# Optimization experiments

Measured on AMD Instinct MI355X. Metric: run time of the kernel, lower is better.

## Reference

```python
import jax, jax.numpy as jnp
import numpy as np

H = 8          # heads
D = 512        # d_model
DK = D // H    # per-head dim
FF = 2048      # feed-forward size
STACKS = 3
VOCAB = 5000
PAD = 0
LN_EPS = 1e-6


def _layer_norm(x, g, b):
    mu = jnp.mean(x, axis=-1, keepdims=True)
    var = jnp.mean(jnp.square(x - mu), axis=-1, keepdims=True)
    return (x - mu) * jax.lax.rsqrt(var + LN_EPS) * g + b


def _positional_encoding(T, d):
    pos = jnp.arange(T, dtype=jnp.float32)[:, None]                      # (T,1)
    div = jnp.exp(jnp.arange(0, d, 2, dtype=jnp.float32) * (-np.log(10000.0) / d))
    pe = jnp.zeros((T, d), dtype=jnp.float32)
    pe = pe.at[:, 0::2].set(jnp.sin(pos * div))
    pe = pe.at[:, 1::2].set(jnp.cos(pos * div))
    return pe  # (T, D)


def _mha(q_in, kv, wq, bq, wk, bk, wv, bv, wo, bo, mask):
    B, Tq, _ = q_in.shape
    Tk = kv.shape[1]
    q = (q_in @ wq + bq).reshape(B, Tq, H, DK).transpose(0, 2, 1, 3)   # (B,H,Tq,DK)
    k = (kv @ wk + bk).reshape(B, Tk, H, DK).transpose(0, 2, 1, 3)
    v = (kv @ wv + bv).reshape(B, Tk, H, DK).transpose(0, 2, 1, 3)
    score = jnp.einsum('bhqd,bhkd->bhqk', q, k) / jnp.sqrt(jnp.float32(DK))
    if mask is not None:
        score = jnp.where(mask, score, jnp.float32(-1e9))
    p = jax.nn.softmax(score, axis=-1)
    out = jnp.einsum('bhqk,bhkd->bhqd', p, v)
    out = out.transpose(0, 2, 1, 3).reshape(B, Tq, D)
    return out @ wo + bo


def setup_inputs() -> dict:
    key = jax.random.key(0)
    ks = jax.random.split(key, 24)
    s = 0.02
    inp = {
        'target': jax.random.randint(ks[0], (32, 256), 0, VOCAB),
        'memory': jax.random.normal(ks[1], (32, 1024, D), dtype=jnp.float32),
        'emb': jax.random.normal(ks[2], (VOCAB, D), dtype=jnp.float32) * s,
        'ln_g': jnp.ones((D,), jnp.float32),
        'ln_b': jnp.zeros((D,), jnp.float32),
        'ff_w1': jax.random.normal(ks[3], (D, FF), jnp.float32) * s,
        'ff_b1': jnp.zeros((FF,), jnp.float32),
        'ff_w2': jax.random.normal(ks[4], (FF, D), jnp.float32) * s,
        'ff_b2': jnp.zeros((D,), jnp.float32),
    }
    names = ['wq', 'wk', 'wv', 'wo']
    for i, n in enumerate(names):
        inp['sa_' + n] = jax.random.normal(ks[5 + i], (D, D), jnp.float32) * s
        inp['sa_b' + n[1]] = jnp.zeros((D,), jnp.float32)
        inp['ca_' + n] = jax.random.normal(ks[9 + i], (D, D), jnp.float32) * s
        inp['ca_b' + n[1]] = jnp.zeros((D,), jnp.float32)
    return inp


def reference(target, memory, emb, ln_g, ln_b, ff_w1, ff_b1, ff_w2, ff_b2,
              sa_wq, sa_bq, sa_wk, sa_bk, sa_wv, sa_bv, sa_wo, sa_bo,
              ca_wq, ca_bq, ca_wk, ca_bk, ca_wv, ca_bv, ca_wo, ca_bo):
    B, T = target.shape
    x = emb[target] * jnp.sqrt(jnp.float32(D))              # (B,T,D)
    x = x + _positional_encoding(T, D)                       # dropout = identity (eval)
    # masks: causal & pad for self-attn; cross-attn mask is all-ones -> skip
    pad = (target != PAD)[:, None, :, None]                  # (B,1,T,1)
    causal = jnp.tril(jnp.ones((T, T), dtype=bool))          # (T,T)
    tgt_mask = pad & causal                                  # (B,1,T,T)
    out = x
    for _ in range(STACKS):  # shared parameters
        n = _layer_norm(out, ln_g, ln_b)
        out = out + _mha(n, n, sa_wq, sa_bq, sa_wk, sa_bk, sa_wv, sa_bv, sa_wo, sa_bo, tgt_mask)
        n = _layer_norm(out, ln_g, ln_b)
        out = out + _mha(n, memory, ca_wq, ca_bq, ca_wk, ca_bk, ca_wv, ca_bv, ca_wo, ca_bo, None)
        n = _layer_norm(out, ln_g, ln_b)
        out = out + (jax.nn.relu(n @ ff_w1 + ff_b1) @ ff_w2 + ff_b2)
    return _layer_norm(out, ln_g, ln_b)
```

## Files before the change

### kernel.cpp

```cpp
#include <hip/hip_runtime.h>
#include <cstdint>
#include <cstddef>

typedef unsigned short u16;
typedef __bf16 bf16x8 __attribute__((ext_vector_type(8)));
typedef float f32x4 __attribute__((ext_vector_type(4)));

#define DEV static __device__ __forceinline__

#define QSCALE 0.18033688011112042f

DEV u16 f2bf(float f) { unsigned v; __builtin_memcpy(&v, &f, 4); v += 0x7fffu + ((v >> 16) & 1u); return (u16)(v >> 16); }

DEV void gll16(const void* g, void* l) {
    __builtin_amdgcn_global_load_lds(
        (__attribute__((address_space(1))) void*)g,
        (__attribute__((address_space(3))) void*)l, 16, 0, 0);
}

__global__ void embed_pe(const int* __restrict__ tgt, const float* __restrict__ emb,
                         float* __restrict__ x)
{
    const int bt = blockIdx.x;
    const int t  = bt & 255;
    const int tok = tgt[bt];
    for (int d = threadIdx.x; d < 512; d += 256) {
        float e  = emb[(size_t)tok * 512 + d] * 22.62741699796952f;
        int   d0 = d & ~1;
        float ang = (float)t * expf((float)d0 * (-9.210340371976184f / 512.f));
        float pe  = (d & 1) ? cosf(ang) : sinf(ang);
        x[(size_t)bt * 512 + d] = e + pe;
    }
}

__global__ void transpose_k(const float* __restrict__ in, u16* __restrict__ out,
                            int K, int N)
{
    int id = blockIdx.x * 256 + threadIdx.x;
    int k = id / N, n = id % N;
    out[(size_t)n * K + k] = f2bf(in[id]);
}

__global__ void memcast(const float* __restrict__ in, u16* __restrict__ out)
{
    int i = (blockIdx.x * 256 + threadIdx.x) * 4;
    float4 v = *(const float4*)(in + i);
    uint2 w;
    w.x = (unsigned)f2bf(v.x) | ((unsigned)f2bf(v.y) << 16);
    w.y = (unsigned)f2bf(v.z) | ((unsigned)f2bf(v.w) << 16);
    *(uint2*)(out + i) = w;
}

__global__ void concat_bias(const float* __restrict__ a, const float* __restrict__ b,
                            float* __restrict__ out)
{
    int i = blockIdx.x * 256 + threadIdx.x;
    if (i < 512) { out[i] = a[i]; out[512 + i] = b[i]; }
}

template<bool OUTF32>
__global__ void layernorm_k(const float* __restrict__ x, const float* __restrict__ g,
                            const float* __restrict__ b, void* __restrict__ outv)
{
    const int row  = blockIdx.x * 4 + (threadIdx.x >> 6);
    const int lane = threadIdx.x & 63;
    const float* xr = x + (size_t)row * 512;
    float4 v0 = *(const float4*)(xr + lane * 4);
    float4 v1 = *(const float4*)(xr + 256 + lane * 4);
    float s = v0.x + v0.y + v0.z + v0.w + v1.x + v1.y + v1.z + v1.w;
    float q = v0.x*v0.x + v0.y*v0.y + v0.z*v0.z + v0.w*v0.w
            + v1.x*v1.x + v1.y*v1.y + v1.z*v1.z + v1.w*v1.w;
#pragma unroll
    for (int o = 1; o < 64; o <<= 1) { s += __shfl_xor(s, o, 64); q += __shfl_xor(q, o, 64); }
    float mu  = s * (1.f / 512.f);
    float var = q * (1.f / 512.f) - mu * mu;
    float rs  = rsqrtf(fmaxf(var, 0.f) + 1e-6f);

#pragma unroll
    for (int h = 0; h < 2; h++) {
        const int d0 = h * 256 + lane * 4;
        float4 v = h ? v1 : v0;
        float4 gg = *(const float4*)(g + d0);
        float4 bb = *(const float4*)(b + d0);
        float o0 = (v.x - mu) * rs * gg.x + bb.x;
        float o1 = (v.y - mu) * rs * gg.y + bb.y;
        float o2 = (v.z - mu) * rs * gg.z + bb.z;
        float o3 = (v.w - mu) * rs * gg.w + bb.w;
        if (OUTF32) {
            *(float4*)((float*)outv + (size_t)row * 512 + d0) = make_float4(o0, o1, o2, o3);
        } else {
            uint2 w;
            w.x = (unsigned)f2bf(o0) | ((unsigned)f2bf(o1) << 16);
            w.y = (unsigned)f2bf(o2) | ((unsigned)f2bf(o3) << 16);
            *(uint2*)((u16*)outv + (size_t)row * 512 + d0) = w;
        }
    }
}

template<bool OUTF32>
__global__ void ln_sum_k(const float* __restrict__ x, const float* __restrict__ p,
                         const float* __restrict__ g, const float* __restrict__ b,
                         float* __restrict__ xout, void* __restrict__ outv)
{
    const int row  = blockIdx.x * 4 + (threadIdx.x >> 6);
    const int lane = threadIdx.x & 63;
    const size_t base = (size_t)row * 512;
    const float* xr = x + base;
    const float* pa = p + base;
    const float* pb = p + 4194304 + base;
    float4 v0, v1;
    {
        float4 a = *(const float4*)(xr + lane * 4);
        float4 c = *(const float4*)(pa + lane * 4);
        float4 d = *(const float4*)(pb + lane * 4);
        v0 = make_float4(a.x + c.x + d.x, a.y + c.y + d.y, a.z + c.z + d.z, a.w + c.w + d.w);
        a = *(const float4*)(xr + 256 + lane * 4);
        c = *(const float4*)(pa + 256 + lane * 4);
        d = *(const float4*)(pb + 256 + lane * 4);
        v1 = make_float4(a.x + c.x + d.x, a.y + c.y + d.y, a.z + c.z + d.z, a.w + c.w + d.w);
    }
    float s = v0.x + v0.y + v0.z + v0.w + v1.x + v1.y + v1.z + v1.w;
    float q = v0.x*v0.x + v0.y*v0.y + v0.z*v0.z + v0.w*v0.w
            + v1.x*v1.x + v1.y*v1.y + v1.z*v1.z + v1.w*v1.w;
#pragma unroll
    for (int o = 1; o < 64; o <<= 1) { s += __shfl_xor(s, o, 64); q += __shfl_xor(q, o, 64); }
    float mu  = s * (1.f / 512.f);
    float var = q * (1.f / 512.f) - mu * mu;
    float rs  = rsqrtf(fmaxf(var, 0.f) + 1e-6f);

#pragma unroll
    for (int h = 0; h < 2; h++) {
        const int d0 = h * 256 + lane * 4;
        float4 v = h ? v1 : v0;
        if (!OUTF32) *(float4*)(xout + base + d0) = v;
        float4 gg = *(const float4*)(g + d0);
        float4 bb = *(const float4*)(b + d0);
        float o0 = (v.x - mu) * rs * gg.x + bb.x;
        float o1 = (v.y - mu) * rs * gg.y + bb.y;
        float o2 = (v.z - mu) * rs * gg.z + bb.z;
        float o3 = (v.w - mu) * rs * gg.w + bb.w;
        if (OUTF32) {
            *(float4*)((float*)outv + base + d0) = make_float4(o0, o1, o2, o3);
        } else {
            uint2 w;
            w.x = (unsigned)f2bf(o0) | ((unsigned)f2bf(o1) << 16);
            w.y = (unsigned)f2bf(o2) | ((unsigned)f2bf(o3) << 16);
            *(uint2*)((u16*)outv + base + d0) = w;
        }
    }
}

template<int EPI, bool BROW, int BN, int QS, int SPLIT>
__launch_bounds__(256, BN == 64 ? 4 : 2)
__global__ void gemm_bt(const u16* __restrict__ A, int lda,
                        const u16* __restrict__ Bt,
                        const float* __restrict__ bias,
                        void* __restrict__ outp, int ldo, int K)
{
    constexpr int NJ = BN / 32;
    __shared__ u16 As[2][128 * 32];
    __shared__ u16 Bs[2][BN * 32];

    const int gx = gridDim.x, gy = gridDim.y;
    const int nwg = gx * gy * gridDim.z;
    int lin = blockIdx.x + gx * (blockIdx.y + gy * blockIdx.z);
    lin = (lin & 7) * (nwg >> 3) + (lin >> 3);
    const int bx = lin % gx;
    const int rem = lin / gx;
    const int by = rem % gy;
    const int bz = rem / gy;

    const int tid  = threadIdx.x;
    const int lane = tid & 63;
    const int wave = tid >> 6;
    const int quad = lane >> 4, l16 = lane & 15;
    const int l4 = lane >> 2, c8 = (lane & 3) * 8;
    const int m0 = by * 128, n0 = bx * BN;
    const int wm = (wave >> 1) * 64, wn = (wave & 1) * (BN / 2);

    const int kc = K / SPLIT;
    const int kbeg = bz * kc;
    const int nsteps = kc / 32;

    f32x4 acc[4][NJ];
#pragma unroll
    for (int i = 0; i < 4; i++)
#pragma unroll
        for (int j = 0; j < NJ; j++) acc[i][j] = f32x4{0.f, 0.f, 0.f, 0.f};

#define GSTAGE(buf, kk)                                                                      \
    {                                                                                        \
        gll16(&A[(size_t)(m0 + wave * 32 + l4)      * lda + (kk) + c8], &As[buf][(wave * 32) * 32]);      \
        gll16(&A[(size_t)(m0 + wave * 32 + 16 + l4) * lda + (kk) + c8], &As[buf][(wave * 32 + 16) * 32]); \
        if (BN == 128) {                                                                     \
            gll16(&Bt[(size_t)(n0 + wave * 32 + l4)      * K + (kk) + c8], &Bs[buf][(wave * 32) * 32]);      \
            gll16(&Bt[(size_t)(n0 + wave * 32 + 16 + l4) * K + (kk) + c8], &Bs[buf][(wave * 32 + 16) * 32]); \
        } else {                                                                             \
            gll16(&Bt[(size_t)(n0 + wave * 16 + l4) * K + (kk) + c8], &Bs[buf][(wave * 16) * 32]);           \
        }                                                                                    \
    }

    GSTAGE(0, kbeg)
    __syncthreads();

    for (int st = 0; st < nsteps; st++) {
        const int cur = st & 1;
        if (st + 1 < nsteps) GSTAGE(cur ^ 1, kbeg + (st + 1) * 32)

        bf16x8 af[4], bfr[NJ];
#pragma unroll
        for (int i = 0; i < 4; i++) af[i]  = *(const bf16x8*)&As[cur][(wm + i * 16 + l16) * 32 + quad * 8];
#pragma unroll
        for (int j = 0; j < NJ; j++) bfr[j] = *(const bf16x8*)&Bs[cur][(wn + j * 16 + l16) * 32 + quad * 8];
#pragma unroll
        for (int i = 0; i < 4; i++)
#pragma unroll
            for (int j = 0; j < NJ; j++)
                acc[i][j] = __builtin_amdgcn_mfma_f32_16x16x32_bf16(af[i], bfr[j], acc[i][j], 0, 0, 0);

        __syncthreads();
    }
#undef GSTAGE

    const bool dobias = (SPLIT == 1) || (bz == 0);
#pragma unroll
    for (int i = 0; i < 4; i++)
#pragma unroll
        for (int j = 0; j < NJ; j++) {
            const int col = n0 + wn + j * 16 + l16;
            const float bc = BROW ? 0.f : (dobias ? bias[col] : 0.f);
#pragma unroll
            for (int r = 0; r < 4; r++) {
                const int row = m0 + wm + i * 16 + quad * 4 + r;
                const float bv = BROW ? (dobias ? bias[row] : 0.f) : bc;
                float v = acc[i][j][r] + bv;
                if (QS == 1) v *= QSCALE;
                if (QS == 2 && col < 512) v *= QSCALE;
                if (EPI == 1) v = fmaxf(v, 0.f);
                if (EPI == 3) {
                    ((float*)outp)[(size_t)bz * 8192 * ldo + (size_t)row * ldo + col] = v;
                } else {
                    ((u16*)outp)[(size_t)row * ldo + col] = f2bf(v);
                }
            }
        }
}

template<bool SELF>
__launch_bounds__(512, 4)
__global__ void attn(const u16* __restrict__ Qb, int qs,
                     const u16* __restrict__ Kb, int ks, int koff,
                     const u16* __restrict__ Vt, int ldv,
                     const int* __restrict__ target,
                     u16* __restrict__ Ob, int Tk)
{
    __shared__ u16 KV[2][4][64 * 32];
    __shared__ __align__(16) __bf16 P16[8][16 * 72];
    __shared__ int needtail;
    const int tid  = threadIdx.x;
    const int lane = tid & 63;
    const int wave = tid >> 6;
    const int quad = lane >> 4, l16 = lane & 15;
    const int b = blockIdx.x, h = blockIdx.y, qz = blockIdx.z;
    const int qbase = qz * 128 + wave * 16;
    const int hq = h * 64;
    const int kcol = ((quad ^ ((l16 >> 1) & 3)) * 8);

    if (tid == 0) needtail = 0;

    const u16* qr = Qb + (size_t)(b * 256 + qbase + l16) * qs + hq;
    bf16x8 qf0 = *(const bf16x8*)(qr + quad * 8);
    bf16x8 qf1 = *(const bf16x8*)(qr + 32 + quad * 8);

    f32x4 o[4];
#pragma unroll
    for (int t = 0; t < 4; t++) o[t] = f32x4{0.f, 0.f, 0.f, 0.f};
    float pr[4] = {0.f, 0.f, 0.f, 0.f};

    bool rv[4];
    bool tpad = false;
    if (SELF) {
        bool inv = false;
#pragma unroll
        for (int r = 0; r < 4; r++) {
            rv[r] = (target[b * 256 + qbase + quad * 4 + r] != 0);
            inv |= !rv[r];
        }
        tpad = __any(inv);
    }

    const u16* kbase = Kb + (size_t)b * Tk * ks + koff + hq;
    const u16* vbase = Vt + (size_t)hq * ldv + (size_t)b * Tk;
    __bf16* pw = P16[wave];

    const int srow0 = ((wave * 2) & 3) * 16 + (lane >> 2);
    const int srow1 = ((wave * 2 + 1) & 3) * 16 + (lane >> 2);
    const int sc0 = (((lane & 3) ^ ((srow0 >> 1) & 3)) * 8);
    const int sc1 = (((lane & 3) ^ ((srow1 >> 1) & 3)) * 8);
    const int arr0 = (wave * 2) >> 2, arr1 = (wave * 2 + 1) >> 2;
    u16* ldst0;  u16* ldst1;

#define STAGE_KV(buf, k0)                                                        \
    {                                                                            \
        const u16* src0; const u16* src1;                                        \
        if (arr0 == 0)      src0 = kbase + (size_t)((k0) + srow0) * ks + sc0;    \
        else if (arr0 == 1) src0 = kbase + (size_t)((k0) + srow0) * ks + 32 + sc0;\
        else if (arr0 == 2) src0 = vbase + (size_t)srow0 * ldv + (k0) + sc0;     \
        else                src0 = vbase + (size_t)srow0 * ldv + (k0) + 32 + sc0;\
        if (arr1 == 0)      src1 = kbase + (size_t)((k0) + srow1) * ks + sc1;    \
        else if (arr1 == 1) src1 = kbase + (size_t)((k0) + srow1) * ks + 32 + sc1;\
        else if (arr1 == 2) src1 = vbase + (size_t)srow1 * ldv + (k0) + sc1;     \
        else                src1 = vbase + (size_t)srow1 * ldv + (k0) + 32 + sc1;\
        ldst0 = &KV[buf][arr0][(((wave * 2) & 3) * 16) * 32];                    \
        ldst1 = &KV[buf][arr1][(((wave * 2 + 1) & 3) * 16) * 32];                \
        gll16(src0, ldst0);                                                      \
        gll16(src1, ldst1);                                                      \
    }

    STAGE_KV(0, 0)
    __syncthreads();
    if (SELF && tpad && lane == 0) needtail = 1;
    __syncthreads();
    const int nch = SELF ? (needtail ? (Tk >> 6) : 2 * (qz + 1)) : (Tk >> 6);

    for (int c = 0; c < nch; c++) {
        const int cur = c & 1;
        const int k0 = c * 64;
        if (c + 1 < nch) STAGE_KV(cur ^ 1, (c + 1) * 64)

        const u16* KsLc = KV[cur][0];
        const u16* KsHc = KV[cur][1];
        const u16* VsLc = KV[cur][2];
        const u16* VsHc = KV[cur][3];

        const bool active = !SELF || (qbase + 16 > k0) || tpad;
        if (active) {
#pragma unroll
            for (int g = 0; g < 4; g++) {
                bf16x8 kf0 = *(const bf16x8*)&KsLc[(g * 16 + l16) * 32 + kcol];
                bf16x8 kf1 = *(const bf16x8*)&KsHc[(g * 16 + l16) * 32 + kcol];
                f32x4 sv = f32x4{0.f, 0.f, 0.f, 0.f};
                sv = __builtin_amdgcn_mfma_f32_16x16x32_bf16(qf0, kf0, sv, 0, 0, 0);
                sv = __builtin_amdgcn_mfma_f32_16x16x32_bf16(qf1, kf1, sv, 0, 0, 0);
                if (SELF) {
                    if (k0 + 64 > qbase) {
#pragma unroll
                        for (int r = 0; r < 4; r++)
                            if (k0 + g * 16 + l16 > qbase + quad * 4 + r) sv[r] = -1e9f;
                    }
                    if (tpad) {
#pragma unroll
                        for (int r = 0; r < 4; r++)
                            if (!rv[r]) sv[r] = 0.f;
                    }
                }
#pragma unroll
                for (int r = 0; r < 4; r++) {
                    float p = exp2f(sv[r]);
                    pr[r] += p;
                    pw[(quad * 4 + r) * 72 + g * 16 + l16] = (__bf16)p;
                }
            }
            bf16x8 pa0 = *(const bf16x8*)&pw[l16 * 72 + quad * 8];
            bf16x8 pa1 = *(const bf16x8*)&pw[l16 * 72 + 32 + quad * 8];
#pragma unroll
            for (int t = 0; t < 4; t++) {
                bf16x8 vf0 = *(const bf16x8*)&VsLc[(t * 16 + l16) * 32 + kcol];
                bf16x8 vf1 = *(const bf16x8*)&VsHc[(t * 16 + l16) * 32 + kcol];
                o[t] = __builtin_amdgcn_mfma_f32_16x16x32_bf16(pa0, vf0, o[t], 0, 0, 0);
                o[t] = __builtin_amdgcn_mfma_f32_16x16x32_bf16(pa1, vf1, o[t], 0, 0, 0);
            }
        }
        __syncthreads();
    }
#undef STAGE_KV

#pragma unroll
    for (int r = 0; r < 4; r++) {
#pragma unroll
        for (int off = 1; off < 16; off <<= 1) pr[r] += __shfl_xor(pr[r], off, 64);
    }
#pragma unroll
    for (int r = 0; r < 4; r++) {
        const float inv_l = 1.f / pr[r];
        const int tq = qbase + quad * 4 + r;
        u16* orow = Ob + (size_t)(b * 256 + tq) * 512 + hq;
#pragma unroll
        for (int t = 0; t < 4; t++) orow[t * 16 + l16] = f2bf(o[t][r] * inv_l);
    }
}

#define O_X      ((size_t)0)
#define O_N      ((size_t)16777216)
#define O_QK     ((size_t)25165824)
#define O_VTS    ((size_t)41943040)
#define O_ATT    ((size_t)50331648)
#define O_FFN    ((size_t)58720256)
#define O_KVC    ((size_t)92274688)
#define O_VTC    ((size_t)125829120)
#define O_WQKT   ((size_t)159383552)
#define O_SAVT   ((size_t)160432128)
#define O_WOT    ((size_t)160956416)
#define O_CAQT   ((size_t)161480704)
#define O_CAKT   ((size_t)162004992)
#define O_CAVT   ((size_t)162529280)
#define O_CAWOT  ((size_t)163053568)
#define O_FF1T   ((size_t)163577856)
#define O_FF2T   ((size_t)165675008)
#define O_BQK    ((size_t)167772160)

extern "C" void kernel_launch(void* const* d_in, const int* in_sizes, int n_in,
                              void* d_out, int out_size, void* d_ws, size_t ws_size,
                              hipStream_t stream)
{
    const int*   target = (const int*)d_in[0];
    const float* memory = (const float*)d_in[1];
    const float* emb    = (const float*)d_in[2];
    const float* ln_g   = (const float*)d_in[3];
    const float* ln_b   = (const float*)d_in[4];
    const float* ff_w1  = (const float*)d_in[5];
    const float* ff_b1  = (const float*)d_in[6];
    const float* ff_w2  = (const float*)d_in[7];
    const float* ff_b2  = (const float*)d_in[8];
    const float* sa_wq  = (const float*)d_in[9];
    const float* sa_bq  = (const float*)d_in[10];
    const float* ca_wq  = (const float*)d_in[11];
    const float* ca_bq  = (const float*)d_in[12];
    const float* sa_wk  = (const float*)d_in[13];
    const float* sa_bk  = (const float*)d_in[14];
    const float* ca_wk  = (const float*)d_in[15];
    const float* ca_bk  = (const float*)d_in[16];
    const float* sa_wv  = (const float*)d_in[17];
    const float* sa_bv  = (const float*)d_in[18];
    const float* ca_wv  = (const float*)d_in[19];
    const float* ca_bv  = (const float*)d_in[20];
    const float* sa_wo  = (const float*)d_in[21];
    const float* sa_bo  = (const float*)d_in[22];
    const float* ca_wo  = (const float*)d_in[23];
    const float* ca_bo  = (const float*)d_in[24];

    char* ws = (char*)d_ws;
    float* xf   = (float*)(ws + O_X);
    u16* nbuf   = (u16*)(ws + O_N);
    u16* qk     = (u16*)(ws + O_QK);
    u16* qbuf   = (u16*)(ws + O_QK);
    float* ffp  = (float*)(ws + O_QK);
    u16* vts    = (u16*)(ws + O_VTS);
    u16* att    = (u16*)(ws + O_ATT);
    u16* ffn    = (u16*)(ws + O_FFN);
    u16* membf  = (u16*)(ws + O_FFN);
    float* wop  = (float*)(ws + O_FFN);
    u16* kvc    = (u16*)(ws + O_KVC);
    u16* vtc    = (u16*)(ws + O_VTC);
    u16* wqkt   = (u16*)(ws + O_WQKT);
    u16* savt   = (u16*)(ws + O_SAVT);
    u16* wot    = (u16*)(ws + O_WOT);
    u16* caqt   = (u16*)(ws + O_CAQT);
    u16* cakt   = (u16*)(ws + O_CAKT);
    u16* cavt   = (u16*)(ws + O_CAVT);
    u16* cawot  = (u16*)(ws + O_CAWOT);
    u16* ff1t   = (u16*)(ws + O_FF1T);
    u16* ff2t   = (u16*)(ws + O_FF2T);
    float* bqk  = (float*)(ws + O_BQK);

    transpose_k<<<1024, 256, 0, stream>>>(sa_wq, wqkt,             512, 512);
    transpose_k<<<1024, 256, 0, stream>>>(sa_wk, wqkt + 512 * 512, 512, 512);
    transpose_k<<<1024, 256, 0, stream>>>(sa_wv, savt,  512, 512);
    transpose_k<<<1024, 256, 0, stream>>>(sa_wo, wot,   512, 512);
    transpose_k<<<1024, 256, 0, stream>>>(ca_wq, caqt,  512, 512);
    transpose_k<<<1024, 256, 0, stream>>>(ca_wk, cakt,  512, 512);
    transpose_k<<<1024, 256, 0, stream>>>(ca_wv, cavt,  512, 512);
    transpose_k<<<1024, 256, 0, stream>>>(ca_wo, cawot, 512, 512);
    transpose_k<<<4096, 256, 0, stream>>>(ff_w1, ff1t,  512, 2048);
    transpose_k<<<4096, 256, 0, stream>>>(ff_w2, ff2t, 2048, 512);
    concat_bias<<<2, 256, 0, stream>>>(sa_bq, sa_bk, bqk);

    embed_pe<<<8192, 256, 0, stream>>>(target, emb, xf);

    memcast<<<16384, 256, 0, stream>>>(memory, membf);
    gemm_bt<0, false, 64, 0, 1><<<dim3(8, 256), 256, 0, stream>>>(membf, 512, cakt, ca_bk, kvc, 512, 512);
    gemm_bt<0, true,  64, 0, 1><<<dim3(512, 4), 256, 0, stream>>>(cavt, 512, membf, ca_bv, vtc, 32768, 512);

    for (int s = 0; s < 3; s++) {
        if (s == 0)
            layernorm_k<false><<<2048, 256, 0, stream>>>(xf, ln_g, ln_b, nbuf);
        else
            ln_sum_k<false><<<2048, 256, 0, stream>>>(xf, ffp, ln_g, ln_b, xf, nbuf);
        gemm_bt<0, false, 64, 2, 1><<<dim3(16, 64), 256, 0, stream>>>(nbuf, 512, wqkt, bqk, qk, 1024, 512);
        gemm_bt<0, true,  64, 0, 1><<<dim3(128, 4), 256, 0, stream>>>(savt, 512, nbuf, sa_bv, vts, 8192, 512);
        attn<true><<<dim3(32, 8, 2), 512, 0, stream>>>(qk, 1024, qk, 1024, 512, vts, 8192, target, att, 256);
        gemm_bt<3, false, 64, 0, 2><<<dim3(8, 64, 2), 256, 0, stream>>>(att, 512, wot, sa_bo, wop, 512, 512);
        ln_sum_k<false><<<2048, 256, 0, stream>>>(xf, wop, ln_g, ln_b, xf, nbuf);
        gemm_bt<0, false, 64, 1, 1><<<dim3(8, 64), 256, 0, stream>>>(nbuf, 512, caqt, ca_bq, qbuf, 512, 512);
        attn<false><<<dim3(32, 8, 2), 512, 0, stream>>>(qbuf, 512, kvc, 512, 0, vtc, 32768, nullptr, att, 1024);
        gemm_bt<3, false, 64, 0, 2><<<dim3(8, 64, 2), 256, 0, stream>>>(att, 512, cawot, ca_bo, wop, 512, 512);
        ln_sum_k<false><<<2048, 256, 0, stream>>>(xf, wop, ln_g, ln_b, xf, nbuf);
        gemm_bt<1, false, 64, 0, 1><<<dim3(32, 64), 256, 0, stream>>>(nbuf, 512, ff1t, ff_b1, ffn, 2048, 512);
        gemm_bt<3, false, 64, 0, 2><<<dim3(8, 64, 2), 256, 0, stream>>>(ffn, 2048, ff2t, ff_b2, ffp, 512, 2048);
    }

    ln_sum_k<true><<<2048, 256, 0, stream>>>(xf, ffp, ln_g, ln_b, xf, d_out);
}
```

Baseline: 916.9 us.

## Shrink attention blocks to 4 waves and load V directly from global

The attention kernel now uses 256-thread blocks covering 64 query rows, with four times as many blocks per launch (z dimension 4). Only K is staged through LDS with async global-to-LDS loads. V fragments are read straight from global memory into registers each chunk. This halves LDS use per block and raises block count, which should improve occupancy and reduce causal-skip waste. The cost is that V is no longer shared through LDS, so it is re-read from global or L2 by each wave, raising memory traffic and adding latency that isn't prefetched.

```diff
diff --git a/kernel.cpp b/kernel.cpp
--- a/kernel.cpp
+++ b/kernel.cpp
@@ -247,22 +247,22 @@
 }
 
 template<bool SELF>
-__launch_bounds__(512, 4)
+__launch_bounds__(256, 4)
 __global__ void attn(const u16* __restrict__ Qb, int qs,
                      const u16* __restrict__ Kb, int ks, int koff,
                      const u16* __restrict__ Vt, int ldv,
                      const int* __restrict__ target,
                      u16* __restrict__ Ob, int Tk)
 {
-    __shared__ u16 KV[2][4][64 * 32];
-    __shared__ __align__(16) __bf16 P16[8][16 * 72];
+    __shared__ u16 Ks[2][2][64 * 32];
+    __shared__ __align__(16) __bf16 P16[4][16 * 72];
     __shared__ int needtail;
     const int tid  = threadIdx.x;
     const int lane = tid & 63;
     const int wave = tid >> 6;
     const int quad = lane >> 4, l16 = lane & 15;
     const int b = blockIdx.x, h = blockIdx.y, qz = blockIdx.z;
-    const int qbase = qz * 128 + wave * 16;
+    const int qbase = qz * 64 + wave * 16;
     const int hq = h * 64;
     const int kcol = ((quad ^ ((l16 >> 1) & 3)) * 8);
 
@@ -293,48 +293,40 @@
     const u16* vbase = Vt + (size_t)hq * ldv + (size_t)b * Tk;
     __bf16* pw = P16[wave];
 
-    const int srow0 = ((wave * 2) & 3) * 16 + (lane >> 2);
-    const int srow1 = ((wave * 2 + 1) & 3) * 16 + (lane >> 2);
-    const int sc0 = (((lane & 3) ^ ((srow0 >> 1) & 3)) * 8);
-    const int sc1 = (((lane & 3) ^ ((srow1 >> 1) & 3)) * 8);
-    const int arr0 = (wave * 2) >> 2, arr1 = (wave * 2 + 1) >> 2;
-    u16* ldst0;  u16* ldst1;
-
-#define STAGE_KV(buf, k0)                                                        \
+    const int sr = lane >> 2;
+    const int sc = (((lane & 3) ^ ((sr >> 1) & 3)) * 8);
+
+#define STAGE_K(buf, k0)                                                         \
     {                                                                            \
-        const u16* src0; const u16* src1;                                        \
-        if (arr0 == 0)      src0 = kbase + (size_t)((k0) + srow0) * ks + sc0;    \
-        else if (arr0 == 1) src0 = kbase + (size_t)((k0) + srow0) * ks + 32 + sc0;\
-        else if (arr0 == 2) src0 = vbase + (size_t)srow0 * ldv + (k0) + sc0;     \
-        else                src0 = vbase + (size_t)srow0 * ldv + (k0) + 32 + sc0;\
-        if (arr1 == 0)      src1 = kbase + (size_t)((k0) + srow1) * ks + sc1;    \
-        else if (arr1 == 1) src1 = kbase + (size_t)((k0) + srow1) * ks + 32 + sc1;\
-        else if (arr1 == 2) src1 = vbase + (size_t)srow1 * ldv + (k0) + sc1;     \
-        else                src1 = vbase + (size_t)srow1 * ldv + (k0) + 32 + sc1;\
-        ldst0 = &KV[buf][arr0][(((wave * 2) & 3) * 16) * 32];                    \
-        ldst1 = &KV[buf][arr1][(((wave * 2 + 1) & 3) * 16) * 32];                \
-        gll16(src0, ldst0);                                                      \
-        gll16(src1, ldst1);                                                      \
-    }
-
-    STAGE_KV(0, 0)
+        gll16(kbase + (size_t)((k0) + wave * 16 + sr) * ks + sc,                 \
+              &Ks[buf][0][(wave * 16) * 32]);                                    \
+        gll16(kbase + (size_t)((k0) + wave * 16 + sr) * ks + 32 + sc,            \
+              &Ks[buf][1][(wave * 16) * 32]);                                    \
+    }
+
+    STAGE_K(0, 0)
     __syncthreads();
     if (SELF && tpad && lane == 0) needtail = 1;
     __syncthreads();
-    const int nch = SELF ? (needtail ? (Tk >> 6) : 2 * (qz + 1)) : (Tk >> 6);
+    const int nch = SELF ? (needtail ? (Tk >> 6) : (qz + 1)) : (Tk >> 6);
 
     for (int c = 0; c < nch; c++) {
         const int cur = c & 1;
         const int k0 = c * 64;
-        if (c + 1 < nch) STAGE_KV(cur ^ 1, (c + 1) * 64)
-
-        const u16* KsLc = KV[cur][0];
-        const u16* KsHc = KV[cur][1];
-        const u16* VsLc = KV[cur][2];
-        const u16* VsHc = KV[cur][3];
+        if (c + 1 < nch) STAGE_K(cur ^ 1, (c + 1) * 64)
+
+        const u16* KsLc = Ks[cur][0];
+        const u16* KsHc = Ks[cur][1];
 
         const bool active = !SELF || (qbase + 16 > k0) || tpad;
         if (active) {
+            bf16x8 vr0[4], vr1[4];
+#pragma unroll
+            for (int t = 0; t < 4; t++) {
+                const u16* vp = vbase + (size_t)(t * 16 + l16) * ldv + k0 + quad * 8;
+                vr0[t] = *(const bf16x8*)vp;
+                vr1[t] = *(const bf16x8*)(vp + 32);
+            }
 #pragma unroll
             for (int g = 0; g < 4; g++) {
                 bf16x8 kf0 = *(const bf16x8*)&KsLc[(g * 16 + l16) * 32 + kcol];
@@ -365,15 +357,13 @@
             bf16x8 pa1 = *(const bf16x8*)&pw[l16 * 72 + 32 + quad * 8];
 #pragma unroll
             for (int t = 0; t < 4; t++) {
-                bf16x8 vf0 = *(const bf16x8*)&VsLc[(t * 16 + l16) * 32 + kcol];
-                bf16x8 vf1 = *(const bf16x8*)&VsHc[(t * 16 + l16) * 32 + kcol];
-                o[t] = __builtin_amdgcn_mfma_f32_16x16x32_bf16(pa0, vf0, o[t], 0, 0, 0);
-                o[t] = __builtin_amdgcn_mfma_f32_16x16x32_bf16(pa1, vf1, o[t], 0, 0, 0);
+                o[t] = __builtin_amdgcn_mfma_f32_16x16x32_bf16(pa0, vr0[t], o[t], 0, 0, 0);
+                o[t] = __builtin_amdgcn_mfma_f32_16x16x32_bf16(pa1, vr1[t], o[t], 0, 0, 0);
             }
         }
         __syncthreads();
     }
-#undef STAGE_KV
+#undef STAGE_K
 
 #pragma unroll
     for (int r = 0; r < 4; r++) {
@@ -488,11 +478,11 @@
             ln_sum_k<false><<<2048, 256, 0, stream>>>(xf, ffp, ln_g, ln_b, xf, nbuf);
         gemm_bt<0, false, 64, 2, 1><<<dim3(16, 64), 256, 0, stream>>>(nbuf, 512, wqkt, bqk, qk, 1024, 512);
         gemm_bt<0, true,  64, 0, 1><<<dim3(128, 4), 256, 0, stream>>>(savt, 512, nbuf, sa_bv, vts, 8192, 512);
-        attn<true><<<dim3(32, 8, 2), 512, 0, stream>>>(qk, 1024, qk, 1024, 512, vts, 8192, target, att, 256);
+        attn<true><<<dim3(32, 8, 4), 256, 0, stream>>>(qk, 1024, qk, 1024, 512, vts, 8192, target, att, 256);
         gemm_bt<3, false, 64, 0, 2><<<dim3(8, 64, 2), 256, 0, stream>>>(att, 512, wot, sa_bo, wop, 512, 512);
         ln_sum_k<false><<<2048, 256, 0, stream>>>(xf, wop, ln_g, ln_b, xf, nbuf);
         gemm_bt<0, false, 64, 1, 1><<<dim3(8, 64), 256, 0, stream>>>(nbuf, 512, caqt, ca_bq, qbuf, 512, 512);
-        attn<false><<<dim3(32, 8, 2), 512, 0, stream>>>(qbuf, 512, kvc, 512, 0, vtc, 32768, nullptr, att, 1024);
+        attn<false><<<dim3(32, 8, 4), 256, 0, stream>>>(qbuf, 512, kvc, 512, 0, vtc, 32768, nullptr, att, 1024);
         gemm_bt<3, false, 64, 0, 2><<<dim3(8, 64, 2), 256, 0, stream>>>(att, 512, cawot, ca_bo, wop, 512, 512);
         ln_sum_k<false><<<2048, 256, 0, stream>>>(xf, wop, ln_g, ln_b, xf, nbuf);
         gemm_bt<1, false, 64, 0, 1><<<dim3(32, 64), 256, 0, stream>>>(nbuf, 512, ff1t, ff_b1, ffn, 2048, 512);
```

New measurement: 1.014 ms. 10.6% more time.

## Process two query tiles per attention block to reuse staged K/V tiles

Applied to the files above, without the earlier changes.

Each attention workgroup now handles two 128-row query tiles (QT=2) instead of one, loading each K/V chunk into LDS once and using it for both tiles. The grid's z dimension drops from 2 to 1, which halves global K/V traffic and the number of blocks. Launch bounds fall from 4 to 2 blocks per CU to make room for the doubled accumulators. The trade-off is fewer blocks (256 total) and lower occupancy. Causal self-attention also loses some skip efficiency, because the first tile now walks every chunk the second tile needs.

```diff
diff --git a/kernel.cpp b/kernel.cpp
--- a/kernel.cpp
+++ b/kernel.cpp
@@ -246,8 +246,8 @@
         }
 }
 
-template<bool SELF>
-__launch_bounds__(512, 4)
+template<bool SELF, int QT>
+__launch_bounds__(512, 2)
 __global__ void attn(const u16* __restrict__ Qb, int qs,
                      const u16* __restrict__ Kb, int ks, int koff,
                      const u16* __restrict__ Vt, int ldv,
@@ -262,31 +262,47 @@
     const int wave = tid >> 6;
     const int quad = lane >> 4, l16 = lane & 15;
     const int b = blockIdx.x, h = blockIdx.y, qz = blockIdx.z;
-    const int qbase = qz * 128 + wave * 16;
     const int hq = h * 64;
     const int kcol = ((quad ^ ((l16 >> 1) & 3)) * 8);
 
     if (tid == 0) needtail = 0;
 
-    const u16* qr = Qb + (size_t)(b * 256 + qbase + l16) * qs + hq;
-    bf16x8 qf0 = *(const bf16x8*)(qr + quad * 8);
-    bf16x8 qf1 = *(const bf16x8*)(qr + 32 + quad * 8);
-
-    f32x4 o[4];
-#pragma unroll
-    for (int t = 0; t < 4; t++) o[t] = f32x4{0.f, 0.f, 0.f, 0.f};
-    float pr[4] = {0.f, 0.f, 0.f, 0.f};
-
-    bool rv[4];
-    bool tpad = false;
+    int qbase[QT];
+    bf16x8 qf0[QT], qf1[QT];
+#pragma unroll
+    for (int i = 0; i < QT; i++) {
+        qbase[i] = qz * (128 * QT) + wave * 16 + i * 128;
+        const u16* qr = Qb + (size_t)(b * 256 + qbase[i] + l16) * qs + hq;
+        qf0[i] = *(const bf16x8*)(qr + quad * 8);
+        qf1[i] = *(const bf16x8*)(qr + 32 + quad * 8);
+    }
+
+    f32x4 o[QT][4];
+#pragma unroll
+    for (int i = 0; i < QT; i++)
+#pragma unroll
+        for (int t = 0; t < 4; t++) o[i][t] = f32x4{0.f, 0.f, 0.f, 0.f};
+    float pr[QT][4];
+#pragma unroll
+    for (int i = 0; i < QT; i++)
+#pragma unroll
+        for (int r = 0; r < 4; r++) pr[i][r] = 0.f;
+
+    bool rv[QT][4];
+    bool tpad[QT];
+    bool anyp = false;
     if (SELF) {
-        bool inv = false;
-#pragma unroll
-        for (int r = 0; r < 4; r++) {
-            rv[r] = (target[b * 256 + qbase + quad * 4 + r] != 0);
-            inv |= !rv[r];
-        }
-        tpad = __any(inv);
+#pragma unroll
+        for (int i = 0; i < QT; i++) {
+            bool inv = false;
+#pragma unroll
+            for (int r = 0; r < 4; r++) {
+                rv[i][r] = (target[b * 256 + qbase[i] + quad * 4 + r] != 0);
+                inv |= !rv[i][r];
+            }
+            tpad[i] = __any(inv);
+            anyp |= tpad[i];
+        }
     }
 
     const u16* kbase = Kb + (size_t)b * Tk * ks + koff + hq;
@@ -319,9 +335,9 @@
 
     STAGE_KV(0, 0)
     __syncthreads();
-    if (SELF && tpad && lane == 0) needtail = 1;
+    if (SELF && anyp && lane == 0) needtail = 1;
     __syncthreads();
-    const int nch = SELF ? (needtail ? (Tk >> 6) : 2 * (qz + 1)) : (Tk >> 6);
+    const int nch = SELF ? (needtail ? (Tk >> 6) : 2 * QT * (qz + 1)) : (Tk >> 6);
 
     for (int c = 0; c < nch; c++) {
         const int cur = c & 1;
@@ -333,42 +349,61 @@
         const u16* VsLc = KV[cur][2];
         const u16* VsHc = KV[cur][3];
 
-        const bool active = !SELF || (qbase + 16 > k0) || tpad;
-        if (active) {
+        bool act[QT];
+        bool anyact = false;
+#pragma unroll
+        for (int i = 0; i < QT; i++) {
+            act[i] = !SELF || (qbase[i] + 16 > k0) || tpad[i];
+            anyact |= act[i];
+        }
+        if (anyact) {
+            bf16x8 kfL[4], kfH[4];
 #pragma unroll
             for (int g = 0; g < 4; g++) {
-                bf16x8 kf0 = *(const bf16x8*)&KsLc[(g * 16 + l16) * 32 + kcol];
-                bf16x8 kf1 = *(const bf16x8*)&KsHc[(g * 16 + l16) * 32 + kcol];
-                f32x4 sv = f32x4{0.f, 0.f, 0.f, 0.f};
-                sv = __builtin_amdgcn_mfma_f32_16x16x32_bf16(qf0, kf0, sv, 0, 0, 0);
-                sv = __builtin_amdgcn_mfma_f32_16x16x32_bf16(qf1, kf1, sv, 0, 0, 0);
-                if (SELF) {
-                    if (k0 + 64 > qbase) {
-#pragma unroll
-                        for (int r = 0; r < 4; r++)
-                            if (k0 + g * 16 + l16 > qbase + quad * 4 + r) sv[r] = -1e9f;
+                kfL[g] = *(const bf16x8*)&KsLc[(g * 16 + l16) * 32 + kcol];
+                kfH[g] = *(const bf16x8*)&KsHc[(g * 16 + l16) * 32 + kcol];
+            }
+            bf16x8 pa0[QT], pa1[QT];
+#pragma unroll
+            for (int i = 0; i < QT; i++) {
+                if (!act[i]) continue;
+#pragma unroll
+                for (int g = 0; g < 4; g++) {
+                    f32x4 sv = f32x4{0.f, 0.f, 0.f, 0.f};
+                    sv = __builtin_amdgcn_mfma_f32_16x16x32_bf16(qf0[i], kfL[g], sv, 0, 0, 0);
+                    sv = __builtin_amdgcn_mfma_f32_16x16x32_bf16(qf1[i], kfH[g], sv, 0, 0, 0);
+                    if (SELF) {
+                        if (k0 + 64 > qbase[i]) {
+#pragma unroll
+                            for (int r = 0; r < 4; r++)
+                                if (k0 + g * 16 + l16 > qbase[i] + quad * 4 + r) sv[r] = -1e9f;
+                        }
+                        if (tpad[i]) {
+#pragma unroll
+                            for (int r = 0; r < 4; r++)
+                                if (!rv[i][r]) sv[r] = 0.f;
+                        }
                     }
-                    if (tpad) {
-#pragma unroll
-                        for (int r = 0; r < 4; r++)
-                            if (!rv[r]) sv[r] = 0.f;
+#pragma unroll
+                    for (int r = 0; r < 4; r++) {
+                        float p = exp2f(sv[r]);
+                        pr[i][r] += p;
+                        pw[(quad * 4 + r) * 72 + g * 16 + l16] = (__bf16)p;
                     }
                 }
-#pragma unroll
-                for (int r = 0; r < 4; r++) {
-                    float p = exp2f(sv[r]);
-                    pr[r] += p;
-                    pw[(quad * 4 + r) * 72 + g * 16 + l16] = (__bf16)p;
-                }
+                pa0[i] = *(const bf16x8*)&pw[l16 * 72 + quad * 8];
+                pa1[i] = *(const bf16x8*)&pw[l16 * 72 + 32 + quad * 8];
             }
-            bf16x8 pa0 = *(const bf16x8*)&pw[l16 * 72 + quad * 8];
-            bf16x8 pa1 = *(const bf16x8*)&pw[l16 * 72 + 32 + quad * 8];
 #pragma unroll
             for (int t = 0; t < 4; t++) {
                 bf16x8 vf0 = *(const bf16x8*)&VsLc[(t * 16 + l16) * 32 + kcol];
                 bf16x8 vf1 = *(const bf16x8*)&VsHc[(t * 16 + l16) * 32 + kcol];
-                o[t] = __builtin_amdgcn_mfma_f32_16x16x32_bf16(pa0, vf0, o[t], 0, 0, 0);
-                o[t] = __builtin_amdgcn_mfma_f32_16x16x32_bf16(pa1, vf1, o[t], 0, 0, 0);
+#pragma unroll
+                for (int i = 0; i < QT; i++) {
+                    if (!act[i]) continue;
+                    o[i][t] = __builtin_amdgcn_mfma_f32_16x16x32_bf16(pa0[i], vf0, o[i][t], 0, 0, 0);
+                    o[i][t] = __builtin_amdgcn_mfma_f32_16x16x32_bf16(pa1[i], vf1, o[i][t], 0, 0, 0);
+                }
             }
         }
         __syncthreads();
@@ -376,17 +411,20 @@
 #undef STAGE_KV
 
 #pragma unroll
-    for (int r = 0; r < 4; r++) {
-#pragma unroll
-        for (int off = 1; off < 16; off <<= 1) pr[r] += __shfl_xor(pr[r], off, 64);
-    }
-#pragma unroll
-    for (int r = 0; r < 4; r++) {
-        const float inv_l = 1.f / pr[r];
-        const int tq = qbase + quad * 4 + r;
-        u16* orow = Ob + (size_t)(b * 256 + tq) * 512 + hq;
-#pragma unroll
-        for (int t = 0; t < 4; t++) orow[t * 16 + l16] = f2bf(o[t][r] * inv_l);
+    for (int i = 0; i < QT; i++) {
+#pragma unroll
+        for (int r = 0; r < 4; r++) {
+#pragma unroll
+            for (int off = 1; off < 16; off <<= 1) pr[i][r] += __shfl_xor(pr[i][r], off, 64);
+        }
+#pragma unroll
+        for (int r = 0; r < 4; r++) {
+            const float inv_l = 1.f / pr[i][r];
+            const int tq = qbase[i] + quad * 4 + r;
+            u16* orow = Ob + (size_t)(b * 256 + tq) * 512 + hq;
+#pragma unroll
+            for (int t = 0; t < 4; t++) orow[t * 16 + l16] = f2bf(o[i][t][r] * inv_l);
+        }
     }
 }
 
@@ -488,11 +526,11 @@
             ln_sum_k<false><<<2048, 256, 0, stream>>>(xf, ffp, ln_g, ln_b, xf, nbuf);
         gemm_bt<0, false, 64, 2, 1><<<dim3(16, 64), 256, 0, stream>>>(nbuf, 512, wqkt, bqk, qk, 1024, 512);
         gemm_bt<0, true,  64, 0, 1><<<dim3(128, 4), 256, 0, stream>>>(savt, 512, nbuf, sa_bv, vts, 8192, 512);
-        attn<true><<<dim3(32, 8, 2), 512, 0, stream>>>(qk, 1024, qk, 1024, 512, vts, 8192, target, att, 256);
+        attn<true, 2><<<dim3(32, 8, 1), 512, 0, stream>>>(qk, 1024, qk, 1024, 512, vts, 8192, target, att, 256);
         gemm_bt<3, false, 64, 0, 2><<<dim3(8, 64, 2), 256, 0, stream>>>(att, 512, wot, sa_bo, wop, 512, 512);
         ln_sum_k<false><<<2048, 256, 0, stream>>>(xf, wop, ln_g, ln_b, xf, nbuf);
         gemm_bt<0, false, 64, 1, 1><<<dim3(8, 64), 256, 0, stream>>>(nbuf, 512, caqt, ca_bq, qbuf, 512, 512);
-        attn<false><<<dim3(32, 8, 2), 512, 0, stream>>>(qbuf, 512, kvc, 512, 0, vtc, 32768, nullptr, att, 1024);
+        attn<false, 2><<<dim3(32, 8, 1), 512, 0, stream>>>(qbuf, 512, kvc, 512, 0, vtc, 32768, nullptr, att, 1024);
         gemm_bt<3, false, 64, 0, 2><<<dim3(8, 64, 2), 256, 0, stream>>>(att, 512, cawot, ca_bo, wop, 512, 512);
         ln_sum_k<false><<<2048, 256, 0, stream>>>(xf, wop, ln_g, ln_b, xf, nbuf);
         gemm_bt<1, false, 64, 0, 1><<<dim3(32, 64), 256, 0, stream>>>(nbuf, 512, ff1t, ff_b1, ffn, 2048, 512);
```

After: 931.5 us. About the same (+1.6%).

## Split cross-attention over key halves with a combine pass; precompute positional table

Applied to the files above, without the earlier changes.

Cross-attention now splits its 1024 keys into two halves handled by separate blocks, doubling the grid. Each block writes unnormalized fp32 numerators and softmax denominators to scratch, and a new combine kernel sums the halves, normalizes and casts to bf16. This targets the under-filled grid of the cross-attention launch but adds a scratch write and read plus one extra launch per stack. Separately, the positional encoding is computed once into a table, so the embedding kernel does vectorized float4 loads instead of running exp/sin/cos per element.

```diff
diff --git a/kernel.cpp b/kernel.cpp
--- a/kernel.cpp
+++ b/kernel.cpp
@@ -18,19 +18,28 @@
         (__attribute__((address_space(3))) void*)l, 16, 0, 0);
 }
 
+__global__ void pe_table(float* __restrict__ pe)
+{
+    const int t = blockIdx.x;
+    for (int d = threadIdx.x; d < 512; d += 256) {
+        const int d0 = d & ~1;
+        float ang = (float)t * expf((float)d0 * (-9.210340371976184f / 512.f));
+        pe[t * 512 + d] = (d & 1) ? cosf(ang) : sinf(ang);
+    }
+}
+
 __global__ void embed_pe(const int* __restrict__ tgt, const float* __restrict__ emb,
-                         float* __restrict__ x)
+                         const float* __restrict__ pe, float* __restrict__ x)
 {
     const int bt = blockIdx.x;
     const int t  = bt & 255;
     const int tok = tgt[bt];
-    for (int d = threadIdx.x; d < 512; d += 256) {
-        float e  = emb[(size_t)tok * 512 + d] * 22.62741699796952f;
-        int   d0 = d & ~1;
-        float ang = (float)t * expf((float)d0 * (-9.210340371976184f / 512.f));
-        float pe  = (d & 1) ? cosf(ang) : sinf(ang);
-        x[(size_t)bt * 512 + d] = e + pe;
-    }
+    const int d = threadIdx.x * 4;
+    float4 e = *(const float4*)(emb + (size_t)tok * 512 + d);
+    float4 p = *(const float4*)(pe + (size_t)t * 512 + d);
+    *(float4*)(x + (size_t)bt * 512 + d) = make_float4(
+        e.x * 22.62741699796952f + p.x, e.y * 22.62741699796952f + p.y,
+        e.z * 22.62741699796952f + p.z, e.w * 22.62741699796952f + p.w);
 }
 
 __global__ void transpose_k(const float* __restrict__ in, u16* __restrict__ out,
@@ -246,13 +255,14 @@
         }
 }
 
-template<bool SELF>
+template<bool SELF, int KS>
 __launch_bounds__(512, 4)
 __global__ void attn(const u16* __restrict__ Qb, int qs,
-                     const u16* __restrict__ Kb, int ks, int koff,
+                     const u16* __restrict__ Kb, int kls, int koff,
                      const u16* __restrict__ Vt, int ldv,
                      const int* __restrict__ target,
-                     u16* __restrict__ Ob, int Tk)
+                     u16* __restrict__ Ob, int Tk,
+                     float* __restrict__ pnum, float* __restrict__ pden)
 {
     __shared__ u16 KV[2][4][64 * 32];
     __shared__ __align__(16) __bf16 P16[8][16 * 72];
@@ -261,10 +271,13 @@
     const int lane = tid & 63;
     const int wave = tid >> 6;
     const int quad = lane >> 4, l16 = lane & 15;
-    const int b = blockIdx.x, h = blockIdx.y, qz = blockIdx.z;
+    const int b = blockIdx.x, h = blockIdx.y;
+    const int qz  = SELF ? blockIdx.z : (blockIdx.z & 1);
+    const int ksp = SELF ? 0 : (blockIdx.z >> 1);
     const int qbase = qz * 128 + wave * 16;
     const int hq = h * 64;
     const int kcol = ((quad ^ ((l16 >> 1) & 3)) * 8);
+    const int c0 = SELF ? 0 : ksp * ((Tk >> 6) / KS);
 
     if (tid == 0) needtail = 0;
 
@@ -289,7 +302,7 @@
         tpad = __any(inv);
     }
 
-    const u16* kbase = Kb + (size_t)b * Tk * ks + koff + hq;
+    const u16* kbase = Kb + (size_t)b * Tk * kls + koff + hq;
     const u16* vbase = Vt + (size_t)hq * ldv + (size_t)b * Tk;
     __bf16* pw = P16[wave];
 
@@ -303,12 +316,12 @@
 #define STAGE_KV(buf, k0)                                                        \
     {                                                                            \
         const u16* src0; const u16* src1;                                        \
-        if (arr0 == 0)      src0 = kbase + (size_t)((k0) + srow0) * ks + sc0;    \
-        else if (arr0 == 1) src0 = kbase + (size_t)((k0) + srow0) * ks + 32 + sc0;\
+        if (arr0 == 0)      src0 = kbase + (size_t)((k0) + srow0) * kls + sc0;   \
+        else if (arr0 == 1) src0 = kbase + (size_t)((k0) + srow0) * kls + 32 + sc0;\
         else if (arr0 == 2) src0 = vbase + (size_t)srow0 * ldv + (k0) + sc0;     \
         else                src0 = vbase + (size_t)srow0 * ldv + (k0) + 32 + sc0;\
-        if (arr1 == 0)      src1 = kbase + (size_t)((k0) + srow1) * ks + sc1;    \
-        else if (arr1 == 1) src1 = kbase + (size_t)((k0) + srow1) * ks + 32 + sc1;\
+        if (arr1 == 0)      src1 = kbase + (size_t)((k0) + srow1) * kls + sc1;   \
+        else if (arr1 == 1) src1 = kbase + (size_t)((k0) + srow1) * kls + 32 + sc1;\
         else if (arr1 == 2) src1 = vbase + (size_t)srow1 * ldv + (k0) + sc1;     \
         else                src1 = vbase + (size_t)srow1 * ldv + (k0) + 32 + sc1;\
         ldst0 = &KV[buf][arr0][(((wave * 2) & 3) * 16) * 32];                    \
@@ -317,16 +330,16 @@
         gll16(src1, ldst1);                                                      \
     }
 
-    STAGE_KV(0, 0)
+    STAGE_KV(0, c0 * 64)
     __syncthreads();
     if (SELF && tpad && lane == 0) needtail = 1;
     __syncthreads();
-    const int nch = SELF ? (needtail ? (Tk >> 6) : 2 * (qz + 1)) : (Tk >> 6);
+    const int nch = SELF ? (needtail ? (Tk >> 6) : 2 * (qz + 1)) : ((Tk >> 6) / KS);
 
     for (int c = 0; c < nch; c++) {
         const int cur = c & 1;
-        const int k0 = c * 64;
-        if (c + 1 < nch) STAGE_KV(cur ^ 1, (c + 1) * 64)
+        const int k0 = (c0 + c) * 64;
+        if (c + 1 < nch) STAGE_KV(cur ^ 1, (c0 + c + 1) * 64)
 
         const u16* KsLc = KV[cur][0];
         const u16* KsHc = KV[cur][1];
@@ -382,12 +395,34 @@
     }
 #pragma unroll
     for (int r = 0; r < 4; r++) {
-        const float inv_l = 1.f / pr[r];
         const int tq = qbase + quad * 4 + r;
-        u16* orow = Ob + (size_t)(b * 256 + tq) * 512 + hq;
-#pragma unroll
-        for (int t = 0; t < 4; t++) orow[t * 16 + l16] = f2bf(o[t][r] * inv_l);
-    }
+        if (KS == 1) {
+            const float inv_l = 1.f / pr[r];
+            u16* orow = Ob + (size_t)(b * 256 + tq) * 512 + hq;
+#pragma unroll
+            for (int t = 0; t < 4; t++) orow[t * 16 + l16] = f2bf(o[t][r] * inv_l);
+        } else {
+            float* np = pnum + (size_t)ksp * 4194304 + (size_t)(b * 256 + tq) * 512 + hq;
+#pragma unroll
+            for (int t = 0; t < 4; t++) np[t * 16 + l16] = o[t][r];
+            if (l16 == 0) pden[(size_t)ksp * 65536 + (size_t)(b * 256 + tq) * 8 + h] = pr[r];
+        }
+    }
+}
+
+__global__ void attn_combine(const float* __restrict__ num, const float* __restrict__ den,
+                             u16* __restrict__ out)
+{
+    const int i = (blockIdx.x * 256 + threadIdx.x) * 4;
+    const int row = i >> 9;
+    const int h = (i >> 6) & 7;
+    const float inv = 1.f / (den[row * 8 + h] + den[65536 + row * 8 + h]);
+    float4 a = *(const float4*)(num + i);
+    float4 c = *(const float4*)(num + 4194304 + i);
+    uint2 w;
+    w.x = (unsigned)f2bf((a.x + c.x) * inv) | ((unsigned)f2bf((a.y + c.y) * inv) << 16);
+    w.y = (unsigned)f2bf((a.z + c.z) * inv) | ((unsigned)f2bf((a.w + c.w) * inv) << 16);
+    *(uint2*)(out + i) = w;
 }
 
 #define O_X      ((size_t)0)
@@ -446,10 +481,13 @@
     u16* qbuf   = (u16*)(ws + O_QK);
     float* ffp  = (float*)(ws + O_QK);
     u16* vts    = (u16*)(ws + O_VTS);
+    float* pef  = (float*)(ws + O_VTS);
+    float* pden = (float*)(ws + O_VTS);
     u16* att    = (u16*)(ws + O_ATT);
     u16* ffn    = (u16*)(ws + O_FFN);
     u16* membf  = (u16*)(ws + O_FFN);
     float* wop  = (float*)(ws + O_FFN);
+    float* pnum = (float*)(ws + O_FFN);
     u16* kvc    = (u16*)(ws + O_KVC);
     u16* vtc    = (u16*)(ws + O_VTC);
     u16* wqkt   = (u16*)(ws + O_WQKT);
@@ -475,7 +513,8 @@
     transpose_k<<<4096, 256, 0, stream>>>(ff_w2, ff2t, 2048, 512);
     concat_bias<<<2, 256, 0, stream>>>(sa_bq, sa_bk, bqk);
 
-    embed_pe<<<8192, 256, 0, stream>>>(target, emb, xf);
+    pe_table<<<256, 256, 0, stream>>>(pef);
+    embed_pe<<<8192, 128, 0, stream>>>(target, emb, pef, xf);
 
     memcast<<<16384, 256, 0, stream>>>(memory, membf);
     gemm_bt<0, false, 64, 0, 1><<<dim3(8, 256), 256, 0, stream>>>(membf, 512, cakt, ca_bk, kvc, 512, 512);
@@ -488,11 +527,12 @@
             ln_sum_k<false><<<2048, 256, 0, stream>>>(xf, ffp, ln_g, ln_b, xf, nbuf);
         gemm_bt<0, false, 64, 2, 1><<<dim3(16, 64), 256, 0, stream>>>(nbuf, 512, wqkt, bqk, qk, 1024, 512);
         gemm_bt<0, true,  64, 0, 1><<<dim3(128, 4), 256, 0, stream>>>(savt, 512, nbuf, sa_bv, vts, 8192, 512);
-        attn<true><<<dim3(32, 8, 2), 512, 0, stream>>>(qk, 1024, qk, 1024, 512, vts, 8192, target, att, 256);
+        attn<true, 1><<<dim3(32, 8, 2), 512, 0, stream>>>(qk, 1024, qk, 1024, 512, vts, 8192, target, att, 256, nullptr, nullptr);
         gemm_bt<3, false, 64, 0, 2><<<dim3(8, 64, 2), 256, 0, stream>>>(att, 512, wot, sa_bo, wop, 512, 512);
         ln_sum_k<false><<<2048, 256, 0, stream>>>(xf, wop, ln_g, ln_b, xf, nbuf);
         gemm_bt<0, false, 64, 1, 1><<<dim3(8, 64), 256, 0, stream>>>(nbuf, 512, caqt, ca_bq, qbuf, 512, 512);
-        attn<false><<<dim3(32, 8, 2), 512, 0, stream>>>(qbuf, 512, kvc, 512, 0, vtc, 32768, nullptr, att, 1024);
+        attn<false, 2><<<dim3(32, 8, 4), 512, 0, stream>>>(qbuf, 512, kvc, 512, 0, vtc, 32768, nullptr, att, 1024, pnum, pden);
+        attn_combine<<<4096, 256, 0, stream>>>(pnum, pden, att);
         gemm_bt<3, false, 64, 0, 2><<<dim3(8, 64, 2), 256, 0, stream>>>(att, 512, cawot, ca_bo, wop, 512, 512);
         ln_sum_k<false><<<2048, 256, 0, stream>>>(xf, wop, ln_g, ln_b, xf, nbuf);
         gemm_bt<1, false, 64, 0, 1><<<dim3(32, 64), 256, 0, stream>>>(nbuf, 512, ff1t, ff_b1, ffn, 2048, 512);
```

Measured after the change: 958.6 us. 4.6% more time.
